# Performance work log

Measured on AMD Instinct MI355X. Metric: run time of the kernel, lower is better.

Reference implementation:

```python
import jax, jax.numpy as jnp
import numpy as np

N = 100000       # nodes
E = 1600000      # edges (avg degree 16)
D = 128          # features_dim = hidden_dim = out_dim
G = 3            # group_num
NUM = 50000      # nodes present in all time groups
ALPHA = 0.2      # LeakyReLU slope
W_SCALE = 0.05


def setup_inputs() -> dict:
    key = jax.random.key(0)
    ks = jax.random.split(key, 8)
    x = jax.random.normal(ks[0], (N, D), jnp.float32)
    edge_index = jax.random.randint(ks[1], (2, E), 0, N, dtype=jnp.int64)
    past = jax.random.normal(ks[2], (G - 1, NUM, D), jnp.float32)
    W1 = jax.random.normal(ks[3], (2 * D, D), jnp.float32) * W_SCALE
    W2 = jax.random.normal(ks[4], (2 * D, D), jnp.float32) * W_SCALE
    W0 = jax.random.normal(ks[5], (D, D), jnp.float32) * W_SCALE
    Wp = jax.random.normal(ks[6], (G - 1, D, D), jnp.float32) * W_SCALE
    W_T = jax.random.normal(ks[7], (2 * D, D), jnp.float32) * W_SCALE
    return {"x": x, "past": past, "W1": W1, "W2": W2, "W0": W0,
            "Wp": Wp, "W_T": W_T, "edge_index": edge_index, "num": NUM}


def reference(x, past, W1, W2, W0, Wp, W_T, edge_index, num):
    src, dst = edge_index[0], edge_index[1]
    n = x.shape[0]
    deg = jax.ops.segment_sum(jnp.ones(src.shape[0], x.dtype), dst, num_segments=n)
    deg = jnp.maximum(deg, 1.0)[:, None]

    def sage_layer(h, W):
        # mean-aggregate neighbors, concat with self, linear + ReLU
        agg = jax.ops.segment_sum(h[src], dst, num_segments=n) / deg
        return jax.nn.relu(jnp.concatenate([h, agg], axis=1) @ W)

    feat = sage_layer(x, W1)      # [N, D]
    feat = sage_layer(feat, W2)   # [N, D]

    # temporal mean aggregation (dropout is identity in eval mode)
    time_feat = (feat[:num] @ W0 + jnp.einsum('knd,kde->ne', past, Wp)) / G
    fused = jnp.concatenate([feat[:num], time_feat], axis=1) @ W_T  # [num, D]
    f = jax.nn.leaky_relu(fused, ALPHA)
    f = f / jnp.maximum(jnp.linalg.norm(f, axis=1, keepdims=True), 1e-12)
    return jnp.concatenate([f, feat[num:]], axis=0)  # [N, D]
```

## Files before the change

### kernel.cpp

```cpp
#include <hip/hip_runtime.h>

#define FD 128
#define CAP 64
#define BSH 8
#define MAXNB 512

typedef __attribute__((ext_vector_type(8))) short bf16x8;
typedef __attribute__((ext_vector_type(4))) float f32x4;

__device__ __forceinline__ float bflo(unsigned v) { return __uint_as_float(v << 16); }
__device__ __forceinline__ float bfhi(unsigned v) { return __uint_as_float(v & 0xffff0000u); }
__device__ __forceinline__ unsigned short f2b(float f) {
  unsigned u = __float_as_uint(f);
  return (unsigned short)((u + 0x7fffu + ((u >> 16) & 1u)) >> 16);
}
__device__ __forceinline__ unsigned pack2(float x, float y) {
  return (unsigned)f2b(x) | ((unsigned)f2b(y) << 16);
}

#if __has_builtin(__builtin_amdgcn_fdot2_f32_bf16)
#define HAVE_DOT2 1
typedef __attribute__((ext_vector_type(2))) __bf16 bf16x2;
__device__ __forceinline__ float dot2acc(unsigned v, unsigned w, float acc) {
  return __builtin_amdgcn_fdot2_f32_bf16(__builtin_bit_cast(bf16x2, v),
                                         __builtin_bit_cast(bf16x2, w), acc, false);
}
#endif

__global__ __launch_bounds__(256) void k_hist(const int* __restrict__ src,
                                              const int* __restrict__ dst,
                                              int* __restrict__ binCnt, int E, int n, int NB) {
  __shared__ int lh[MAXNB];
  for (int i = threadIdx.x; i < NB; i += 256) lh[i] = 0;
  __syncthreads();
  for (int e = blockIdx.x * 256 + threadIdx.x; e < E; e += gridDim.x * 256) {
    unsigned s = (unsigned)src[e], d = (unsigned)dst[e];
    if (s < (unsigned)n && d < (unsigned)n) atomicAdd(&lh[d >> BSH], 1);
  }
  __syncthreads();
  for (int i = threadIdx.x; i < NB; i += 256) {
    int c = lh[i];
    if (c) atomicAdd(&binCnt[i], c);
  }
}

__global__ __launch_bounds__(512) void k_scan(const int* __restrict__ binCnt,
                                              int* __restrict__ binStart,
                                              int* __restrict__ binCur, int NB) {
  __shared__ int buf[512];
  int t = threadIdx.x;
  int v0 = (t < NB) ? binCnt[t] : 0;
  buf[t] = v0;
  __syncthreads();
  for (int off = 1; off < 512; off <<= 1) {
    int v = (t >= off) ? buf[t - off] : 0;
    __syncthreads();
    buf[t] += v;
    __syncthreads();
  }
  if (t < NB) {
    int ex = buf[t] - v0;
    binStart[t] = ex;
    binCur[t] = ex;
  }
}

__global__ __launch_bounds__(256) void k_binscatter(const int* __restrict__ src,
                                                    const int* __restrict__ dst,
                                                    int* __restrict__ binCur,
                                                    uint2* __restrict__ binned, int E, int n, int NB) {
  __shared__ int lcnt[MAXNB], lbase[MAXNB];
  const int CH = 4096;
  int e0 = blockIdx.x * CH;
  for (int i = threadIdx.x; i < NB; i += 256) lcnt[i] = 0;
  __syncthreads();
  int se[16], de[16];
#pragma unroll
  for (int k = 0; k < 16; ++k) {
    int e = e0 + k * 256 + threadIdx.x;
    int ok = e < E;
    unsigned s = ok ? (unsigned)src[e] : 0u;
    unsigned d = ok ? (unsigned)dst[e] : 0u;
    ok = ok && s < (unsigned)n && d < (unsigned)n;
    se[k] = (int)s;
    de[k] = ok ? (int)d : -1;
    if (ok) atomicAdd(&lcnt[d >> BSH], 1);
  }
  __syncthreads();
  for (int i = threadIdx.x; i < NB; i += 256) {
    int c = lcnt[i];
    lbase[i] = c ? atomicAdd(&binCur[i], c) : 0;
    lcnt[i] = 0;
  }
  __syncthreads();
#pragma unroll
  for (int k = 0; k < 16; ++k) {
    if (de[k] >= 0) {
      int b = de[k] >> BSH;
      int p = lbase[b] + atomicAdd(&lcnt[b], 1);
      binned[p] = make_uint2((unsigned)se[k], (unsigned)de[k]);
    }
  }
}

__global__ __launch_bounds__(256) void k_bucket2(const uint2* __restrict__ binned,
                                                 const int* __restrict__ binStart,
                                                 const int* __restrict__ binCnt,
                                                 int* __restrict__ cnt,
                                                 int* __restrict__ idx, int n) {
  __shared__ int lcnt[256];
  int bin = blockIdx.x;
  int base = bin << BSH;
  lcnt[threadIdx.x] = 0;
  __syncthreads();
  int s0 = binStart[bin], c0 = binCnt[bin];
  for (int i = threadIdx.x; i < c0; i += 256) {
    uint2 pr = binned[s0 + i];
    int p = atomicAdd(&lcnt[pr.y & 255], 1);
    if (p < CAP) idx[(size_t)pr.y * CAP + p] = (int)pr.x;
  }
  __syncthreads();
  int d = base + threadIdx.x;
  if (d < n) cnt[d] = lcnt[threadIdx.x];
}

__global__ __launch_bounds__(256) void k_xcast(const float4* __restrict__ x,
                                               unsigned short* __restrict__ xb, int total4) {
  int i = blockIdx.x * 256 + threadIdx.x;
  if (i >= total4) return;
  float4 v = x[i];
  *(uint2*)&xb[(size_t)i * 4] = make_uint2(pack2(v.x, v.y), pack2(v.z, v.w));
}

__global__ __launch_bounds__(64) void k_wpack(const float* __restrict__ W,
                                              unsigned short* __restrict__ Wf, int KROWS) {
  int nkt = KROWS >> 5;
  int ct = blockIdx.x % 8, kt = blockIdx.x / 8;
  int lane = threadIdx.x;
  int m = lane & 15, q = lane >> 4;
  int nn = ct * 16 + m;
  int k0 = kt * 32 + q * 8;
  unsigned short tmp[8];
#pragma unroll
  for (int j = 0; j < 8; ++j) tmp[j] = f2b(W[(size_t)(k0 + j) * FD + nn]);
  unsigned short* dst = Wf + ((size_t)(ct * nkt + kt) * 64 + lane) * 8;
  *(uint4*)dst = *(uint4*)tmp;
}

__global__ __launch_bounds__(64) void k_wpack3(const float* __restrict__ W0,
                                               const float* __restrict__ WpA,
                                               const float* __restrict__ WpB,
                                               unsigned short* __restrict__ Wf) {
  int ct = blockIdx.x % 8, kt = blockIdx.x / 8;
  const float* src = kt < 4 ? W0 : (kt < 8 ? WpA : WpB);
  int ktl = kt & 3;
  int lane = threadIdx.x;
  int m = lane & 15, q = lane >> 4;
  int nn = ct * 16 + m;
  int k0 = ktl * 32 + q * 8;
  unsigned short tmp[8];
#pragma unroll
  for (int j = 0; j < 8; ++j) tmp[j] = f2b(src[(size_t)(k0 + j) * FD + nn]);
  unsigned short* dst = Wf + ((size_t)(ct * 12 + kt) * 64 + lane) * 8;
  *(uint4*)dst = *(uint4*)tmp;
}

template <int OUT_BF16>
__global__ __launch_bounds__(256) void k_sage(const unsigned* __restrict__ hb,
                                              const int* __restrict__ cnt,
                                              const int* __restrict__ idx,
                                              const unsigned short* __restrict__ Wf,
                                              float* __restrict__ outf,
                                              unsigned short* __restrict__ outb, int n) {
  __shared__ unsigned short sa[32][264];
  int tid = threadIdx.x;
  int lane = tid & 63, wv = tid >> 6;
  int rowBase = blockIdx.x * 32;

  for (int i = tid; i < 32 * 64; i += 256) {
    int r = i >> 6, cp = i & 63;
    int gr = rowBase + r;
    unsigned v = (gr < n) ? hb[(size_t)gr * 64 + cp] : 0u;
    *(unsigned*)&sa[r][cp * 2] = v;
  }

  int rbase = wv * 8;
  const int* ip = idx + (size_t)(rowBase + rbase) * CAP;
  int vidx[8];
  int c[8];
  int maxc = 0;
#pragma unroll
  for (int j = 0; j < 8; ++j) {
    int gr = rowBase + rbase + j;
    int cj = (gr < n) ? min(cnt[gr], CAP) : 0;
    cj = __builtin_amdgcn_readfirstlane(cj);
    c[j] = cj;
    maxc = max(maxc, cj);
    int v = 0;
    if (lane < cj) v = ip[j * CAP + lane];
    vidx[j] = v;
  }

#ifdef HAVE_DOT2
  float sxa[8], dxa[8];
#pragma unroll
  for (int j = 0; j < 8; ++j) { sxa[j] = 0.f; dxa[j] = 0.f; }
  const unsigned ONES = 0x3F803F80u;
  const unsigned PMON = 0xBF803F80u;

  for (int e = 0; e < maxc; e += 2) {
    int e1 = min(e + 1, CAP - 1);
#pragma unroll
    for (int j = 0; j < 8; ++j) {
      int s0 = __builtin_amdgcn_readlane(vidx[j], e);
      int s1 = __builtin_amdgcn_readlane(vidx[j], e1);
      s0 = (e < c[j]) ? s0 : n;
      s1 = (e + 1 < c[j]) ? s1 : n;
      unsigned v0 = hb[(size_t)s0 * 64 + lane];
      unsigned v1 = hb[(size_t)s1 * 64 + lane];
      sxa[j] = dot2acc(v0, ONES, sxa[j]);
      sxa[j] = dot2acc(v1, ONES, sxa[j]);
      dxa[j] = dot2acc(v0, PMON, dxa[j]);
      dxa[j] = dot2acc(v1, PMON, dxa[j]);
    }
  }
#pragma unroll
  for (int j = 0; j < 8; ++j) {
    float inv = 0.5f / fmaxf((float)c[j], 1.0f);
    float ax = (sxa[j] + dxa[j]) * inv;
    float ay = (sxa[j] - dxa[j]) * inv;
    *(unsigned*)&sa[rbase + j][FD + lane * 2] = pack2(ax, ay);
  }
#else
  float ax[8], ay[8];
#pragma unroll
  for (int j = 0; j < 8; ++j) { ax[j] = 0.f; ay[j] = 0.f; }

  for (int e = 0; e < maxc; e += 2) {
    int e1 = min(e + 1, CAP - 1);
#pragma unroll
    for (int j = 0; j < 8; ++j) {
      int s0 = __builtin_amdgcn_readlane(vidx[j], e);
      int s1 = __builtin_amdgcn_readlane(vidx[j], e1);
      s0 = (e < c[j]) ? s0 : n;
      s1 = (e + 1 < c[j]) ? s1 : n;
      unsigned v0 = hb[(size_t)s0 * 64 + lane];
      unsigned v1 = hb[(size_t)s1 * 64 + lane];
      ax[j] += bflo(v0) + bflo(v1);
      ay[j] += bfhi(v0) + bfhi(v1);
    }
  }
#pragma unroll
  for (int j = 0; j < 8; ++j) {
    float inv = 1.0f / fmaxf((float)c[j], 1.0f);
    *(unsigned*)&sa[rbase + j][FD + lane * 2] = pack2(ax[j] * inv, ay[j] * inv);
  }
#endif
  __syncthreads();

  int m = lane & 15, q = lane >> 4;
  f32x4 z = {0.f, 0.f, 0.f, 0.f};
  f32x4 acc[2][2] = {{z, z}, {z, z}};
  int ct0 = wv * 2;
  const bf16x8* WfV = (const bf16x8*)Wf;
#pragma unroll
  for (int kt = 0; kt < 8; ++kt) {
    bf16x8 a0 = *(const bf16x8*)&sa[m][kt * 32 + q * 8];
    bf16x8 a1 = *(const bf16x8*)&sa[16 + m][kt * 32 + q * 8];
    bf16x8 b0 = WfV[(size_t)(ct0 * 8 + kt) * 64 + lane];
    bf16x8 b1 = WfV[(size_t)((ct0 + 1) * 8 + kt) * 64 + lane];
    acc[0][0] = __builtin_amdgcn_mfma_f32_16x16x32_bf16(a0, b0, acc[0][0], 0, 0, 0);
    acc[0][1] = __builtin_amdgcn_mfma_f32_16x16x32_bf16(a0, b1, acc[0][1], 0, 0, 0);
    acc[1][0] = __builtin_amdgcn_mfma_f32_16x16x32_bf16(a1, b0, acc[1][0], 0, 0, 0);
    acc[1][1] = __builtin_amdgcn_mfma_f32_16x16x32_bf16(a1, b1, acc[1][1], 0, 0, 0);
  }

#pragma unroll
  for (int rt = 0; rt < 2; ++rt) {
#pragma unroll
    for (int t = 0; t < 2; ++t) {
      int col = (ct0 + t) * 16 + m;
#pragma unroll
      for (int reg = 0; reg < 4; ++reg) {
        int gr = rowBase + rt * 16 + q * 4 + reg;
        if (gr < n) {
          float v = fmaxf(acc[rt][t][reg], 0.f);
          if (OUT_BF16)
            outb[(size_t)gr * FD + col] = f2b(v);
          else
            outf[(size_t)gr * FD + col] = v;
        }
      }
    }
  }
}

__global__ __launch_bounds__(256) void k_fuse(const float* __restrict__ feat2,
                                              const float* __restrict__ past,
                                              const unsigned short* __restrict__ Wcf,
                                              const unsigned short* __restrict__ Wtf,
                                              float* __restrict__ out, int num) {
  __shared__ unsigned short sa[32][392];
  __shared__ float so[32][132];
  int tid = threadIdx.x;
  int lane = tid & 63, wv = tid >> 6;
  int base = blockIdx.x * 32;

  for (int i = tid; i < 32 * 64; i += 256) {
    int r = i >> 6, cp = i & 63;
    int gr = base + r;
    float2 vf = {0.f, 0.f}, v0 = {0.f, 0.f}, v1 = {0.f, 0.f};
    if (gr < num) {
      vf = *(const float2*)&feat2[(size_t)gr * FD + cp * 2];
      v0 = *(const float2*)&past[(size_t)gr * FD + cp * 2];
      v1 = *(const float2*)&past[(size_t)num * FD + (size_t)gr * FD + cp * 2];
    }
    *(unsigned*)&sa[r][cp * 2]       = pack2(vf.x, vf.y);
    *(unsigned*)&sa[r][FD + cp * 2]  = pack2(v0.x, v0.y);
    *(unsigned*)&sa[r][256 + cp * 2] = pack2(v1.x, v1.y);
  }
  __syncthreads();

  int m = lane & 15, q = lane >> 4;
  int ct0 = wv * 2;
  f32x4 z = {0.f, 0.f, 0.f, 0.f};
  const bf16x8* WcV = (const bf16x8*)Wcf;
  const bf16x8* WtV = (const bf16x8*)Wtf;

  f32x4 acc[2][2] = {{z, z}, {z, z}};
#pragma unroll
  for (int kt = 0; kt < 12; ++kt) {
    bf16x8 a0 = *(const bf16x8*)&sa[m][kt * 32 + q * 8];
    bf16x8 a1 = *(const bf16x8*)&sa[16 + m][kt * 32 + q * 8];
    bf16x8 b0 = WcV[(size_t)(ct0 * 12 + kt) * 64 + lane];
    bf16x8 b1 = WcV[(size_t)((ct0 + 1) * 12 + kt) * 64 + lane];
    acc[0][0] = __builtin_amdgcn_mfma_f32_16x16x32_bf16(a0, b0, acc[0][0], 0, 0, 0);
    acc[0][1] = __builtin_amdgcn_mfma_f32_16x16x32_bf16(a0, b1, acc[0][1], 0, 0, 0);
    acc[1][0] = __builtin_amdgcn_mfma_f32_16x16x32_bf16(a1, b0, acc[1][0], 0, 0, 0);
    acc[1][1] = __builtin_amdgcn_mfma_f32_16x16x32_bf16(a1, b1, acc[1][1], 0, 0, 0);
  }
  __syncthreads();

  const float inv3 = 1.0f / 3.0f;
#pragma unroll
  for (int rt = 0; rt < 2; ++rt)
#pragma unroll
    for (int t = 0; t < 2; ++t) {
      int col = (ct0 + t) * 16 + m;
#pragma unroll
      for (int reg = 0; reg < 4; ++reg)
        sa[rt * 16 + q * 4 + reg][FD + col] = f2b(acc[rt][t][reg] * inv3);
    }
  __syncthreads();

  f32x4 acc2[2][2] = {{z, z}, {z, z}};
#pragma unroll
  for (int kt = 0; kt < 8; ++kt) {
    bf16x8 a0 = *(const bf16x8*)&sa[m][kt * 32 + q * 8];
    bf16x8 a1 = *(const bf16x8*)&sa[16 + m][kt * 32 + q * 8];
    bf16x8 b0 = WtV[(size_t)(ct0 * 8 + kt) * 64 + lane];
    bf16x8 b1 = WtV[(size_t)((ct0 + 1) * 8 + kt) * 64 + lane];
    acc2[0][0] = __builtin_amdgcn_mfma_f32_16x16x32_bf16(a0, b0, acc2[0][0], 0, 0, 0);
    acc2[0][1] = __builtin_amdgcn_mfma_f32_16x16x32_bf16(a0, b1, acc2[0][1], 0, 0, 0);
    acc2[1][0] = __builtin_amdgcn_mfma_f32_16x16x32_bf16(a1, b0, acc2[1][0], 0, 0, 0);
    acc2[1][1] = __builtin_amdgcn_mfma_f32_16x16x32_bf16(a1, b1, acc2[1][1], 0, 0, 0);
  }

#pragma unroll
  for (int rt = 0; rt < 2; ++rt)
#pragma unroll
    for (int t = 0; t < 2; ++t) {
      int col = (ct0 + t) * 16 + m;
#pragma unroll
      for (int reg = 0; reg < 4; ++reg) {
        float v = acc2[rt][t][reg];
        so[rt * 16 + q * 4 + reg][col] = v > 0.f ? v : 0.2f * v;
      }
    }
  __syncthreads();

#pragma unroll
  for (int j = 0; j < 8; ++j) {
    int r = wv * 8 + j;
    float v0 = so[r][lane * 2], v1 = so[r][lane * 2 + 1];
    float ss = v0 * v0 + v1 * v1;
#pragma unroll
    for (int mk = 32; mk >= 1; mk >>= 1) ss += __shfl_xor(ss, mk, 64);
    float inv = 1.0f / fmaxf(sqrtf(ss), 1e-12f);
    int gr = base + r;
    if (gr < num) {
      float2 o = {v0 * inv, v1 * inv};
      *(float2*)&out[(size_t)gr * FD + lane * 2] = o;
    }
  }
}

extern "C" void kernel_launch(void* const* d_in, const int* in_sizes, int n_in,
                              void* d_out, int out_size, void* d_ws, size_t ws_size,
                              hipStream_t stream) {
  const float* x    = (const float*)d_in[0];
  const float* past = (const float*)d_in[1];
  const float* W1   = (const float*)d_in[2];
  const float* W2   = (const float*)d_in[3];
  const float* W0   = (const float*)d_in[4];
  const float* Wp   = (const float*)d_in[5];
  const float* WT   = (const float*)d_in[6];
  const int*   ei   = (const int*)d_in[7];

  int N   = in_sizes[0] / FD;
  int NUM = in_sizes[1] / (2 * FD);
  int E   = in_sizes[7] / 2;
  const int* src = ei;
  const int* dst = ei + E;
  float* out = (float*)d_out;

  int NB = (N + 255) >> BSH;

  char* p = (char*)d_ws;
  int* cnt      = (int*)p;  p += (((size_t)N * 4 + 255) & ~(size_t)255);
  int* idx      = (int*)p;  p += (size_t)N * CAP * 4;
  int* binCnt   = (int*)p;  p += MAXNB * 4;
  int* binStart = (int*)p;  p += MAXNB * 4;
  int* binCur   = (int*)p;  p += MAXNB * 4;
  uint2* binned = (uint2*)p; p += (size_t)E * 8;
  unsigned short* xb  = (unsigned short*)p; p += (size_t)(N + 1) * FD * 2;
  unsigned short* f1b = (unsigned short*)p; p += (size_t)(N + 1) * FD * 2;
  unsigned short* w1f = (unsigned short*)p; p += (size_t)8 * 8 * 64 * 8 * 2;
  unsigned short* w2f = (unsigned short*)p; p += (size_t)8 * 8 * 64 * 8 * 2;
  unsigned short* wcf = (unsigned short*)p; p += (size_t)8 * 12 * 64 * 8 * 2;
  unsigned short* wtf = (unsigned short*)p;

  hipMemsetAsync(binCnt, 0, MAXNB * sizeof(int), stream);
  hipMemsetAsync(xb + (size_t)N * FD, 0, FD * 2, stream);
  hipMemsetAsync(f1b + (size_t)N * FD, 0, FD * 2, stream);

  k_hist<<<400, 256, 0, stream>>>(src, dst, binCnt, E, N, NB);
  k_scan<<<1, 512, 0, stream>>>(binCnt, binStart, binCur, NB);
  k_binscatter<<<(E + 4095) / 4096, 256, 0, stream>>>(src, dst, binCur, binned, E, N, NB);
  k_bucket2<<<NB, 256, 0, stream>>>(binned, binStart, binCnt, cnt, idx, N);

  k_xcast<<<(N * 32 + 255) / 256, 256, 0, stream>>>((const float4*)x, xb, N * 32);
  k_wpack<<<64, 64, 0, stream>>>(W1, w1f, 2 * FD);
  k_wpack<<<64, 64, 0, stream>>>(W2, w2f, 2 * FD);
  k_wpack3<<<96, 64, 0, stream>>>(W0, Wp, Wp + FD * FD, wcf);
  k_wpack<<<64, 64, 0, stream>>>(WT, wtf, 2 * FD);

  int sageGrid = (N + 31) / 32;
  k_sage<1><<<sageGrid, 256, 0, stream>>>((const unsigned*)xb, cnt, idx, w1f, nullptr, f1b, N);
  k_sage<0><<<sageGrid, 256, 0, stream>>>((const unsigned*)f1b, cnt, idx, w2f, out, nullptr, N);
  k_fuse<<<(NUM + 31) / 32, 256, 0, stream>>>(out, past, wcf, wtf, out, NUM);
}
```

Measured before the change: 401.0 us.

## Pack binned edges to 32 bits, unroll gathers, pass bf16 feat2 to fuse

Edge binning now stores one packed 32-bit word (low 8 bits of dst plus a 24-bit src) instead of a uint2, which halves binned traffic. The histogram reads only dst. The second SAGE layer writes rows below NUM as bf16 into the reused xb buffer, so the fuse kernel reads bf16 instead of fp32 feat2, and those rows of out are written only once as the final result. The neighbor gather loops are unrolled to 4 edges per iteration for more memory-level parallelism, and the self-row load is widened. The packing assumes node ids fit in 24 bits, and out-of-range src ids are clamped to 0 instead of dropping the edge.

```diff
diff --git a/kernel.cpp b/kernel.cpp
--- a/kernel.cpp
+++ b/kernel.cpp
@@ -27,15 +27,14 @@
 }
 #endif
 
-__global__ __launch_bounds__(256) void k_hist(const int* __restrict__ src,
-                                              const int* __restrict__ dst,
+__global__ __launch_bounds__(256) void k_hist(const int* __restrict__ dst,
                                               int* __restrict__ binCnt, int E, int n, int NB) {
   __shared__ int lh[MAXNB];
   for (int i = threadIdx.x; i < NB; i += 256) lh[i] = 0;
   __syncthreads();
   for (int e = blockIdx.x * 256 + threadIdx.x; e < E; e += gridDim.x * 256) {
-    unsigned s = (unsigned)src[e], d = (unsigned)dst[e];
-    if (s < (unsigned)n && d < (unsigned)n) atomicAdd(&lh[d >> BSH], 1);
+    unsigned d = (unsigned)dst[e];
+    if (d < (unsigned)n) atomicAdd(&lh[d >> BSH], 1);
   }
   __syncthreads();
   for (int i = threadIdx.x; i < NB; i += 256) {
@@ -68,7 +67,7 @@
 __global__ __launch_bounds__(256) void k_binscatter(const int* __restrict__ src,
                                                     const int* __restrict__ dst,
                                                     int* __restrict__ binCur,
-                                                    uint2* __restrict__ binned, int E, int n, int NB) {
+                                                    unsigned* __restrict__ binned, int E, int n, int NB) {
   __shared__ int lcnt[MAXNB], lbase[MAXNB];
   const int CH = 4096;
   int e0 = blockIdx.x * CH;
@@ -81,7 +80,8 @@
     int ok = e < E;
     unsigned s = ok ? (unsigned)src[e] : 0u;
     unsigned d = ok ? (unsigned)dst[e] : 0u;
-    ok = ok && s < (unsigned)n && d < (unsigned)n;
+    if (s >= (unsigned)n) s = 0;
+    ok = ok && d < (unsigned)n;
     se[k] = (int)s;
     de[k] = ok ? (int)d : -1;
     if (ok) atomicAdd(&lcnt[d >> BSH], 1);
@@ -98,12 +98,12 @@
     if (de[k] >= 0) {
       int b = de[k] >> BSH;
       int p = lbase[b] + atomicAdd(&lcnt[b], 1);
-      binned[p] = make_uint2((unsigned)se[k], (unsigned)de[k]);
-    }
-  }
-}
-
-__global__ __launch_bounds__(256) void k_bucket2(const uint2* __restrict__ binned,
+      binned[p] = ((unsigned)(de[k] & 255) << 24) | (unsigned)se[k];
+    }
+  }
+}
+
+__global__ __launch_bounds__(256) void k_bucket2(const unsigned* __restrict__ binned,
                                                  const int* __restrict__ binStart,
                                                  const int* __restrict__ binCnt,
                                                  int* __restrict__ cnt,
@@ -115,9 +115,10 @@
   __syncthreads();
   int s0 = binStart[bin], c0 = binCnt[bin];
   for (int i = threadIdx.x; i < c0; i += 256) {
-    uint2 pr = binned[s0 + i];
-    int p = atomicAdd(&lcnt[pr.y & 255], 1);
-    if (p < CAP) idx[(size_t)pr.y * CAP + p] = (int)pr.x;
+    unsigned pr = binned[s0 + i];
+    int dlow = (int)(pr >> 24);
+    int p = atomicAdd(&lcnt[dlow], 1);
+    if (p < CAP) idx[(size_t)(base + dlow) * CAP + p] = (int)(pr & 0xFFFFFFu);
   }
   __syncthreads();
   int d = base + threadIdx.x;
@@ -165,23 +166,23 @@
   *(uint4*)dst = *(uint4*)tmp;
 }
 
-template <int OUT_BF16>
 __global__ __launch_bounds__(256) void k_sage(const unsigned* __restrict__ hb,
                                               const int* __restrict__ cnt,
                                               const int* __restrict__ idx,
                                               const unsigned short* __restrict__ Wf,
                                               float* __restrict__ outf,
-                                              unsigned short* __restrict__ outb, int n) {
+                                              unsigned short* __restrict__ outb,
+                                              int nbThr, int n) {
   __shared__ unsigned short sa[32][264];
   int tid = threadIdx.x;
   int lane = tid & 63, wv = tid >> 6;
   int rowBase = blockIdx.x * 32;
 
-  for (int i = tid; i < 32 * 64; i += 256) {
-    int r = i >> 6, cp = i & 63;
+  for (int i = tid; i < 32 * 32; i += 256) {
+    int r = i >> 5, cp = i & 31;
     int gr = rowBase + r;
-    unsigned v = (gr < n) ? hb[(size_t)gr * 64 + cp] : 0u;
-    *(unsigned*)&sa[r][cp * 2] = v;
+    uint2 v = (gr < n) ? *(const uint2*)&hb[(size_t)gr * 64 + cp * 2] : make_uint2(0u, 0u);
+    *(uint2*)&sa[r][cp * 4] = v;
   }
 
   int rbase = wv * 8;
@@ -208,20 +209,31 @@
   const unsigned ONES = 0x3F803F80u;
   const unsigned PMON = 0xBF803F80u;
 
-  for (int e = 0; e < maxc; e += 2) {
-    int e1 = min(e + 1, CAP - 1);
+  for (int e = 0; e < maxc; e += 4) {
+    int l1 = min(e + 1, CAP - 1), l2 = min(e + 2, CAP - 1), l3 = min(e + 3, CAP - 1);
+    unsigned v[8][4];
 #pragma unroll
     for (int j = 0; j < 8; ++j) {
       int s0 = __builtin_amdgcn_readlane(vidx[j], e);
-      int s1 = __builtin_amdgcn_readlane(vidx[j], e1);
-      s0 = (e < c[j]) ? s0 : n;
+      int s1 = __builtin_amdgcn_readlane(vidx[j], l1);
+      int s2 = __builtin_amdgcn_readlane(vidx[j], l2);
+      int s3 = __builtin_amdgcn_readlane(vidx[j], l3);
+      s0 = (e     < c[j]) ? s0 : n;
       s1 = (e + 1 < c[j]) ? s1 : n;
-      unsigned v0 = hb[(size_t)s0 * 64 + lane];
-      unsigned v1 = hb[(size_t)s1 * 64 + lane];
-      sxa[j] = dot2acc(v0, ONES, sxa[j]);
-      sxa[j] = dot2acc(v1, ONES, sxa[j]);
-      dxa[j] = dot2acc(v0, PMON, dxa[j]);
-      dxa[j] = dot2acc(v1, PMON, dxa[j]);
+      s2 = (e + 2 < c[j]) ? s2 : n;
+      s3 = (e + 3 < c[j]) ? s3 : n;
+      v[j][0] = hb[(size_t)s0 * 64 + lane];
+      v[j][1] = hb[(size_t)s1 * 64 + lane];
+      v[j][2] = hb[(size_t)s2 * 64 + lane];
+      v[j][3] = hb[(size_t)s3 * 64 + lane];
+    }
+#pragma unroll
+    for (int j = 0; j < 8; ++j) {
+#pragma unroll
+      for (int k = 0; k < 4; ++k) {
+        sxa[j] = dot2acc(v[j][k], ONES, sxa[j]);
+        dxa[j] = dot2acc(v[j][k], PMON, dxa[j]);
+      }
     }
   }
 #pragma unroll
@@ -236,18 +248,31 @@
 #pragma unroll
   for (int j = 0; j < 8; ++j) { ax[j] = 0.f; ay[j] = 0.f; }
 
-  for (int e = 0; e < maxc; e += 2) {
-    int e1 = min(e + 1, CAP - 1);
+  for (int e = 0; e < maxc; e += 4) {
+    int l1 = min(e + 1, CAP - 1), l2 = min(e + 2, CAP - 1), l3 = min(e + 3, CAP - 1);
+    unsigned v[8][4];
 #pragma unroll
     for (int j = 0; j < 8; ++j) {
       int s0 = __builtin_amdgcn_readlane(vidx[j], e);
-      int s1 = __builtin_amdgcn_readlane(vidx[j], e1);
-      s0 = (e < c[j]) ? s0 : n;
+      int s1 = __builtin_amdgcn_readlane(vidx[j], l1);
+      int s2 = __builtin_amdgcn_readlane(vidx[j], l2);
+      int s3 = __builtin_amdgcn_readlane(vidx[j], l3);
+      s0 = (e     < c[j]) ? s0 : n;
       s1 = (e + 1 < c[j]) ? s1 : n;
-      unsigned v0 = hb[(size_t)s0 * 64 + lane];
-      unsigned v1 = hb[(size_t)s1 * 64 + lane];
-      ax[j] += bflo(v0) + bflo(v1);
-      ay[j] += bfhi(v0) + bfhi(v1);
+      s2 = (e + 2 < c[j]) ? s2 : n;
+      s3 = (e + 3 < c[j]) ? s3 : n;
+      v[j][0] = hb[(size_t)s0 * 64 + lane];
+      v[j][1] = hb[(size_t)s1 * 64 + lane];
+      v[j][2] = hb[(size_t)s2 * 64 + lane];
+      v[j][3] = hb[(size_t)s3 * 64 + lane];
+    }
+#pragma unroll
+    for (int j = 0; j < 8; ++j) {
+#pragma unroll
+      for (int k = 0; k < 4; ++k) {
+        ax[j] += bflo(v[j][k]);
+        ay[j] += bfhi(v[j][k]);
+      }
     }
   }
 #pragma unroll
@@ -285,7 +310,7 @@
         int gr = rowBase + rt * 16 + q * 4 + reg;
         if (gr < n) {
           float v = fmaxf(acc[rt][t][reg], 0.f);
-          if (OUT_BF16)
+          if (gr < nbThr)
             outb[(size_t)gr * FD + col] = f2b(v);
           else
             outf[(size_t)gr * FD + col] = v;
@@ -295,7 +320,7 @@
   }
 }
 
-__global__ __launch_bounds__(256) void k_fuse(const float* __restrict__ feat2,
+__global__ __launch_bounds__(256) void k_fuse(const unsigned short* __restrict__ feat2b,
                                               const float* __restrict__ past,
                                               const unsigned short* __restrict__ Wcf,
                                               const unsigned short* __restrict__ Wtf,
@@ -306,16 +331,18 @@
   int lane = tid & 63, wv = tid >> 6;
   int base = blockIdx.x * 32;
 
+  const unsigned* f2u = (const unsigned*)feat2b;
   for (int i = tid; i < 32 * 64; i += 256) {
     int r = i >> 6, cp = i & 63;
     int gr = base + r;
-    float2 vf = {0.f, 0.f}, v0 = {0.f, 0.f}, v1 = {0.f, 0.f};
+    unsigned uvf = 0u;
+    float2 v0 = {0.f, 0.f}, v1 = {0.f, 0.f};
     if (gr < num) {
-      vf = *(const float2*)&feat2[(size_t)gr * FD + cp * 2];
+      uvf = f2u[(size_t)gr * 64 + cp];
       v0 = *(const float2*)&past[(size_t)gr * FD + cp * 2];
       v1 = *(const float2*)&past[(size_t)num * FD + (size_t)gr * FD + cp * 2];
     }
-    *(unsigned*)&sa[r][cp * 2]       = pack2(vf.x, vf.y);
+    *(unsigned*)&sa[r][cp * 2]       = uvf;
     *(unsigned*)&sa[r][FD + cp * 2]  = pack2(v0.x, v0.y);
     *(unsigned*)&sa[r][256 + cp * 2] = pack2(v1.x, v1.y);
   }
@@ -422,19 +449,20 @@
   int* binCnt   = (int*)p;  p += MAXNB * 4;
   int* binStart = (int*)p;  p += MAXNB * 4;
   int* binCur   = (int*)p;  p += MAXNB * 4;
-  uint2* binned = (uint2*)p; p += (size_t)E * 8;
+  unsigned* binned = (unsigned*)p; p += (size_t)E * 4;
   unsigned short* xb  = (unsigned short*)p; p += (size_t)(N + 1) * FD * 2;
   unsigned short* f1b = (unsigned short*)p; p += (size_t)(N + 1) * FD * 2;
   unsigned short* w1f = (unsigned short*)p; p += (size_t)8 * 8 * 64 * 8 * 2;
   unsigned short* w2f = (unsigned short*)p; p += (size_t)8 * 8 * 64 * 8 * 2;
   unsigned short* wcf = (unsigned short*)p; p += (size_t)8 * 12 * 64 * 8 * 2;
   unsigned short* wtf = (unsigned short*)p;
+  unsigned short* f2b = xb;
 
   hipMemsetAsync(binCnt, 0, MAXNB * sizeof(int), stream);
   hipMemsetAsync(xb + (size_t)N * FD, 0, FD * 2, stream);
   hipMemsetAsync(f1b + (size_t)N * FD, 0, FD * 2, stream);
 
-  k_hist<<<400, 256, 0, stream>>>(src, dst, binCnt, E, N, NB);
+  k_hist<<<400, 256, 0, stream>>>(dst, binCnt, E, N, NB);
   k_scan<<<1, 512, 0, stream>>>(binCnt, binStart, binCur, NB);
   k_binscatter<<<(E + 4095) / 4096, 256, 0, stream>>>(src, dst, binCur, binned, E, N, NB);
   k_bucket2<<<NB, 256, 0, stream>>>(binned, binStart, binCnt, cnt, idx, N);
@@ -446,7 +474,7 @@
   k_wpack<<<64, 64, 0, stream>>>(WT, wtf, 2 * FD);
 
   int sageGrid = (N + 31) / 32;
-  k_sage<1><<<sageGrid, 256, 0, stream>>>((const unsigned*)xb, cnt, idx, w1f, nullptr, f1b, N);
-  k_sage<0><<<sageGrid, 256, 0, stream>>>((const unsigned*)f1b, cnt, idx, w2f, out, nullptr, N);
-  k_fuse<<<(NUM + 31) / 32, 256, 0, stream>>>(out, past, wcf, wtf, out, NUM);
-}
+  k_sage<<<sageGrid, 256, 0, stream>>>((const unsigned*)xb, cnt, idx, w1f, nullptr, f1b, N, N);
+  k_sage<<<sageGrid, 256, 0, stream>>>((const unsigned*)f1b, cnt, idx, w2f, out, f2b, NUM, N);
+  k_fuse<<<(NUM + 31) / 32, 256, 0, stream>>>(f2b, past, wcf, wtf, out, NUM);
+}
```

Measured after the change: 400.4 us. About the same (-0.1%).
